# Optimization experiments

Measured on AMD Instinct MI355X. Metric: run time of the kernel, lower is better.

Reference implementation:

```python
import jax, jax.numpy as jnp
import numpy as np
from jax import lax

IN_C, OUT_C, K, Z_DIM, GROUPS = 256, 256, 3, 64, 1
B, H, W = 16, 32, 32


def setup_inputs() -> dict:
    key = jax.random.key(0)
    k1, k2, k3 = jax.random.split(key, 3)
    x = jax.random.normal(k1, (B, IN_C, H, W), dtype=jnp.float32)
    z = jax.random.normal(k2, (B, Z_DIM), dtype=jnp.float32)
    # nn.Linear(z_dim, groups*out_per_group*in_per_group*k*k, bias=False).weight
    fan = GROUPS * (OUT_C // GROUPS) * (IN_C // GROUPS) * K * K  # 589824
    w_lin = jax.random.normal(k3, (fan, Z_DIM), dtype=jnp.float32) * (1.0 / np.sqrt(Z_DIM))
    return {"x": x, "z": z, "w_lin": w_lin}


def reference(x, z, w_lin):
    b = x.shape[0]
    in_per_group = IN_C // GROUPS
    # hypernetwork: per-sample conv weights [B, out_c, in_c/groups, k, k]
    Wgen = (z @ w_lin.T).reshape(b, OUT_C, in_per_group, K, K)
    pad = K // 2

    def conv_one(xi, Wi):
        # xi: [in_c, H, W], Wi: [out_c, in_c/groups, k, k]
        y = lax.conv_general_dilated(
            xi[None], Wi,
            window_strides=(1, 1),
            padding=[(pad, pad), (pad, pad)],
            dimension_numbers=("NCHW", "OIHW", "NCHW"),
            feature_group_count=GROUPS,
        )
        return y[0]

    return jax.vmap(conv_one)(x, Wgen)  # [B, out_c, H, W]
```

## Files before the change

kernel.cpp:

```cpp
#include <hip/hip_runtime.h>

#define PB_ 589824
#define XT_PB 295936
#define XGR 544

typedef __bf16 bf16;
typedef __bf16 bf16x4 __attribute__((ext_vector_type(4)));
typedef __bf16 bf16x8 __attribute__((ext_vector_type(8)));
typedef float f32x4 __attribute__((ext_vector_type(4)));

static __device__ inline bf16x8 cvt8(float4 a, float4 b) {
  bf16x8 r;
  r[0] = (bf16)a.x; r[1] = (bf16)a.y; r[2] = (bf16)a.z; r[3] = (bf16)a.w;
  r[4] = (bf16)b.x; r[5] = (bf16)b.y; r[6] = (bf16)b.z; r[7] = (bf16)b.w;
  return r;
}

__global__ __launch_bounds__(256) void prep_kernel(const float* __restrict__ z,
                                                   const float* __restrict__ wl,
                                                   const float* __restrict__ x,
                                                   bf16* __restrict__ WgA,
                                                   bf16* __restrict__ xt) {
  const int bid = blockIdx.x;
  if (bid < 1152) {
    __shared__ __align__(16) char wsm[16384];
    const int c_  = bid & 7;
    const int tap = (bid >> 3) % 9;
    const int ob  = bid / 72;
    const int lane = threadIdx.x & 63;
    const int wave = threadIdx.x >> 6;
    const int l15 = lane & 15;
    const int q = lane >> 4;

    const float* zp = z + l15 * 64 + q * 8;
    bf16x8 bz[2];
#pragma unroll
    for (int kc = 0; kc < 2; ++kc)
      bz[kc] = cvt8(*(const float4*)(zp + kc * 32), *(const float4*)(zp + kc * 32 + 4));

#pragma unroll
    for (int mi = 0; mi < 4; ++mi) {
      const int m = wave * 4 + mi;
#pragma unroll
      for (int h = 0; h < 2; ++h) {
        const long t = (long)(ob * 16 + m) * 2304 + (c_ * 32 + h * 16 + l15) * 9 + tap;
        const float* wp = wl + t * 64 + q * 8;
        f32x4 acc = {0.f, 0.f, 0.f, 0.f};
#pragma unroll
        for (int kc = 0; kc < 2; ++kc) {
          bf16x8 aw = cvt8(*(const float4*)(wp + kc * 32), *(const float4*)(wp + kc * 32 + 4));
          acc = __builtin_amdgcn_mfma_f32_16x16x32_bf16(aw, bz[kc], acc, 0, 0, 0);
        }
        bf16x4 o;
        o[0] = (bf16)acc[0]; o[1] = (bf16)acc[1]; o[2] = (bf16)acc[2]; o[3] = (bf16)acc[3];
        const int elem = ((h * 2 + (q >> 1)) * 16 + m) * 8 + (q & 1) * 4;
        int byte = (l15 << 10) + elem * 2;
        byte ^= (l15 & 7) << 4;
        *(bf16x4*)(wsm + byte) = o;
      }
    }
    __syncthreads();
    const int b = threadIdx.x >> 4;
    const int l16 = threadIdx.x & 15;
    const long gbase = ((((long)b * 16 + ob) * 9 + tap) * 8 + c_) * 512;
#pragma unroll
    for (int i = 0; i < 4; ++i) {
      int byte = (b << 10) + (l16 << 4) + (i << 8);
      byte ^= (b & 7) << 4;
      uint4 v = *(const uint4*)(wsm + byte);
      *(uint4*)(WgA + gbase + l16 * 8 + i * 128) = v;
    }
  } else if (bid < 1416) {
    int g = (bid - 1152) * 256 + threadIdx.x;
    int b = g / 4224;
    int rem = g - b * 4224;
    int pi = rem >> 5;
    int gq = rem & 31;
    int p;
    if (pi < 34) p = pi;
    else if (pi < 68) p = 1122 + (pi - 34);
    else {
      int k = (pi - 68) >> 1;
      p = (k + 1) * 34 + (((pi - 68) & 1) ? 33 : 0);
    }
    *(uint4*)(xt + (long)b * XT_PB + p * 256 + gq * 8) = make_uint4(0u, 0u, 0u, 0u);
  } else {
    __shared__ bf16 tile[32][33];
    int i = bid - 1416;
    int row = i & 31, c0 = ((i >> 5) & 7) * 32, b = i >> 8;
    int l = threadIdx.x & 31;
    int r = threadIdx.x >> 5;
#pragma unroll
    for (int j = 0; j < 4; ++j) {
      int ch = r + j * 8;
      tile[ch][l] = (bf16)x[((b * 256 + c0 + ch) * 1024) + row * 32 + l];
    }
    __syncthreads();
#pragma unroll
    for (int j = 0; j < 4; ++j) {
      int col = r + j * 8;
      xt[(long)b * XT_PB + ((row + 1) * 34 + (col + 1)) * 256 + c0 + l] = tile[l][col];
    }
  }
}

__global__ __launch_bounds__(256, 4) void conv_kernel(const bf16* __restrict__ WgA,
                                                      const bf16* __restrict__ xt,
                                                      float* __restrict__ y) {
  __shared__ __align__(16) bf16 xs[2][XGR * 8];
  const int id = blockIdx.x;
  const int xcd = id & 7;
  const int k = id >> 3;
  const int b = ((k & 1) << 3) | xcd;
  const int r2 = k >> 1;
  const int mt = r2 & 3;
  const int nt = r2 >> 2;
  const int tid = threadIdx.x;
  const int lane = tid & 63;
  const int wave = tid >> 6;
  const int wm = wave & 1;
  const int wn = wave >> 1;
  const int l15 = lane & 15;
  const int q = lane >> 4;
  const int oc0 = mt * 64;

  const bf16* xtb = xt + (long)b * XT_PB;
  const bf16* xstage = xtb + (nt * 2) * 34 * 256;
  const bf16* Wb = WgA + (long)b * PB_;

  f32x4 acc[2][2] = {};

#define STAGE(IC0, SEL)                                                          \
  for (int g0 = wave * 64; g0 < XGR; g0 += 256) {                                \
    int g = g0 + lane;                                                           \
    int pix = g >> 2, slot = g & 3;                                              \
    int qq = slot ^ ((pix >> 1) & 3);                                            \
    if (g < XGR) {                                                               \
      const bf16* src = xstage + (pix * 256 + (IC0) + qq * 8);                   \
      __builtin_amdgcn_global_load_lds(                                          \
          (const __attribute__((address_space(1))) void*)src,                    \
          (__attribute__((address_space(3))) void*)(&xs[SEL][g0 * 8]), 16, 0, 0);\
    }                                                                            \
  }

  STAGE(0, 0)
  for (int c = 0; c < 8; ++c) {
    __syncthreads();
    if (c < 7) { STAGE((c + 1) * 32, (c + 1) & 1) }
    const bf16* buf = &xs[c & 1][0];
#pragma unroll
    for (int tap = 0; tap < 9; ++tap) {
      const int kh = tap / 3, kw = tap % 3;
      bf16x8 afr[2];
#pragma unroll
      for (int mi = 0; mi < 2; ++mi) {
        const int ob = (oc0 >> 4) + wm * 2 + mi;
        afr[mi] = *(const bf16x8*)(Wb + (((ob * 9 + tap) * 8 + c) * 512 + lane * 8));
      }
      bf16x8 bfr[2];
#pragma unroll
      for (int n = 0; n < 2; ++n) {
        int pl = wn * 32 + n * 16;
        int pr = pl >> 5;
        int pc = (pl & 31) + l15;
        int spix = (pr + kh) * 34 + pc + kw;
        bfr[n] = *(const bf16x8*)(buf + spix * 32 + ((((spix >> 1) & 3) ^ q) * 8));
      }
#pragma unroll
      for (int mi = 0; mi < 2; ++mi)
#pragma unroll
        for (int n = 0; n < 2; ++n)
          acc[mi][n] = __builtin_amdgcn_mfma_f32_16x16x32_bf16(afr[mi], bfr[n],
                                                               acc[mi][n], 0, 0, 0);
    }
  }

#pragma unroll
  for (int mi = 0; mi < 2; ++mi) {
    int ocb = oc0 + (wm * 2 + mi) * 16 + q * 4;
#pragma unroll
    for (int n = 0; n < 2; ++n) {
      int p = nt * 64 + wn * 32 + n * 16 + l15;
      float* yp = y + ((long)b * 256 + ocb) * 1024 + p;
#pragma unroll
      for (int rr = 0; rr < 4; ++rr)
        yp[rr * 1024] = acc[mi][n][rr];
    }
  }
#undef STAGE
}

extern "C" void kernel_launch(void* const* d_in, const int* in_sizes, int n_in,
                              void* d_out, int out_size, void* d_ws, size_t ws_size,
                              hipStream_t stream) {
  const float* x  = (const float*)d_in[0];
  const float* z  = (const float*)d_in[1];
  const float* wl = (const float*)d_in[2];
  float* y = (float*)d_out;
  bf16* WgA = (bf16*)d_ws;
  bf16* xt  = (bf16*)((char*)d_ws + 18874368);

  prep_kernel<<<5512, 256, 0, stream>>>(z, wl, x, WgA, xt);
  conv_kernel<<<1024, 256, 0, stream>>>(WgA, xt, y);
}
```

Before: 261.7 us.

## Fuse prep and conv into a persistent kernel with a grid-wide barrier

Merges the weight-generation and input-transpose prep kernel with the convolution kernel into one persistent launch of 1024 blocks. The blocks loop over the prep work items, meet at an atomic-counter grid barrier, then each runs its conv tile. This is meant to remove the second kernel launch and the tail gap between the two kernels. It adds a tiny zero-counter launch and a spin barrier, which deadlocks if all 1024 blocks cannot be resident at once. It also cuts prep parallelism from 5512 blocks to 1024 looping blocks.

```diff
diff --git a/kernel.cpp b/kernel.cpp
--- a/kernel.cpp
+++ b/kernel.cpp
@@ -3,6 +3,9 @@
 #define PB_ 589824
 #define XT_PB 295936
 #define XGR 544
+#define NBLK 1024
+#define NPREP 5512
+#define CTR_OFF 28344320
 
 typedef __bf16 bf16;
 typedef __bf16 bf16x4 __attribute__((ext_vector_type(4)));
@@ -16,178 +19,193 @@
   return r;
 }
 
-__global__ __launch_bounds__(256) void prep_kernel(const float* __restrict__ z,
-                                                   const float* __restrict__ wl,
-                                                   const float* __restrict__ x,
-                                                   bf16* __restrict__ WgA,
-                                                   bf16* __restrict__ xt) {
-  const int bid = blockIdx.x;
-  if (bid < 1152) {
-    __shared__ __align__(16) char wsm[16384];
-    const int c_  = bid & 7;
-    const int tap = (bid >> 3) % 9;
-    const int ob  = bid / 72;
-    const int lane = threadIdx.x & 63;
-    const int wave = threadIdx.x >> 6;
+__global__ void zero_ctr(unsigned* c) { *c = 0u; }
+
+__global__ __launch_bounds__(256, 4) void fused_kernel(const float* __restrict__ z,
+                                                       const float* __restrict__ wl,
+                                                       const float* __restrict__ x,
+                                                       bf16* __restrict__ WgA,
+                                                       bf16* __restrict__ xt,
+                                                       float* __restrict__ y,
+                                                       unsigned* __restrict__ ctr) {
+  __shared__ __align__(16) char smem[17408];
+  const int g = blockIdx.x;
+  const int tid = threadIdx.x;
+
+  for (int u = g; u < NPREP; u += NBLK) {
+    if (u < 1152) {
+      char* wsm = smem;
+      const int c_  = u & 7;
+      const int tap = (u >> 3) % 9;
+      const int ob  = u / 72;
+      const int lane = tid & 63;
+      const int wave = tid >> 6;
+      const int l15 = lane & 15;
+      const int q = lane >> 4;
+
+      const float* zp = z + l15 * 64 + q * 8;
+      bf16x8 bz[2];
+#pragma unroll
+      for (int kc = 0; kc < 2; ++kc)
+        bz[kc] = cvt8(*(const float4*)(zp + kc * 32), *(const float4*)(zp + kc * 32 + 4));
+
+#pragma unroll
+      for (int mi = 0; mi < 4; ++mi) {
+        const int m = wave * 4 + mi;
+#pragma unroll
+        for (int h = 0; h < 2; ++h) {
+          const long t = (long)(ob * 16 + m) * 2304 + (c_ * 32 + h * 16 + l15) * 9 + tap;
+          const float* wp = wl + t * 64 + q * 8;
+          f32x4 acc = {0.f, 0.f, 0.f, 0.f};
+#pragma unroll
+          for (int kc = 0; kc < 2; ++kc) {
+            bf16x8 aw = cvt8(*(const float4*)(wp + kc * 32), *(const float4*)(wp + kc * 32 + 4));
+            acc = __builtin_amdgcn_mfma_f32_16x16x32_bf16(aw, bz[kc], acc, 0, 0, 0);
+          }
+          bf16x4 o;
+          o[0] = (bf16)acc[0]; o[1] = (bf16)acc[1]; o[2] = (bf16)acc[2]; o[3] = (bf16)acc[3];
+          const int elem = ((h * 2 + (q >> 1)) * 16 + m) * 8 + (q & 1) * 4;
+          int byte = (l15 << 10) + elem * 2;
+          byte ^= (l15 & 7) << 4;
+          *(bf16x4*)(wsm + byte) = o;
+        }
+      }
+      __syncthreads();
+      const int bb = tid >> 4;
+      const int l16 = tid & 15;
+      const long gbase = ((((long)bb * 16 + ob) * 9 + tap) * 8 + c_) * 512;
+#pragma unroll
+      for (int i = 0; i < 4; ++i) {
+        int byte = (bb << 10) + (l16 << 4) + (i << 8);
+        byte ^= (bb & 7) << 4;
+        uint4 v = *(const uint4*)(wsm + byte);
+        *(uint4*)(WgA + gbase + l16 * 8 + i * 128) = v;
+      }
+    } else if (u < 1416) {
+      int gg = (u - 1152) * 256 + tid;
+      int b = gg / 4224;
+      int rem = gg - b * 4224;
+      int pi = rem >> 5;
+      int gq = rem & 31;
+      int p;
+      if (pi < 34) p = pi;
+      else if (pi < 68) p = 1122 + (pi - 34);
+      else {
+        int kk = (pi - 68) >> 1;
+        p = (kk + 1) * 34 + (((pi - 68) & 1) ? 33 : 0);
+      }
+      *(uint4*)(xt + (long)b * XT_PB + p * 256 + gq * 8) = make_uint4(0u, 0u, 0u, 0u);
+    } else {
+      bf16(*tile)[33] = (bf16(*)[33])smem;
+      int i = u - 1416;
+      int row = i & 31, c0 = ((i >> 5) & 7) * 32, b = i >> 8;
+      int l = tid & 31;
+      int r = tid >> 5;
+#pragma unroll
+      for (int j = 0; j < 4; ++j) {
+        int ch = r + j * 8;
+        tile[ch][l] = (bf16)x[((b * 256 + c0 + ch) * 1024) + row * 32 + l];
+      }
+      __syncthreads();
+#pragma unroll
+      for (int j = 0; j < 4; ++j) {
+        int col = r + j * 8;
+        xt[(long)b * XT_PB + ((row + 1) * 34 + (col + 1)) * 256 + c0 + l] = tile[l][col];
+      }
+    }
+    __syncthreads();
+  }
+
+  if (tid == 0) {
+    __hip_atomic_fetch_add(ctr, 1u, __ATOMIC_RELEASE, __HIP_MEMORY_SCOPE_AGENT);
+    while (__hip_atomic_load(ctr, __ATOMIC_ACQUIRE, __HIP_MEMORY_SCOPE_AGENT) < NBLK)
+      __builtin_amdgcn_s_sleep(16);
+  }
+  __syncthreads();
+
+  {
+    bf16* xsb = (bf16*)smem;
+    const int id = g;
+    const int xcd = id & 7;
+    const int k = id >> 3;
+    const int b = ((k & 1) << 3) | xcd;
+    const int r2 = k >> 1;
+    const int mt = r2 & 3;
+    const int nt = r2 >> 2;
+    const int lane = tid & 63;
+    const int wave = tid >> 6;
+    const int wm = wave & 1;
+    const int wn = wave >> 1;
     const int l15 = lane & 15;
     const int q = lane >> 4;
-
-    const float* zp = z + l15 * 64 + q * 8;
-    bf16x8 bz[2];
-#pragma unroll
-    for (int kc = 0; kc < 2; ++kc)
-      bz[kc] = cvt8(*(const float4*)(zp + kc * 32), *(const float4*)(zp + kc * 32 + 4));
-
-#pragma unroll
-    for (int mi = 0; mi < 4; ++mi) {
-      const int m = wave * 4 + mi;
-#pragma unroll
-      for (int h = 0; h < 2; ++h) {
-        const long t = (long)(ob * 16 + m) * 2304 + (c_ * 32 + h * 16 + l15) * 9 + tap;
-        const float* wp = wl + t * 64 + q * 8;
-        f32x4 acc = {0.f, 0.f, 0.f, 0.f};
-#pragma unroll
-        for (int kc = 0; kc < 2; ++kc) {
-          bf16x8 aw = cvt8(*(const float4*)(wp + kc * 32), *(const float4*)(wp + kc * 32 + 4));
-          acc = __builtin_amdgcn_mfma_f32_16x16x32_bf16(aw, bz[kc], acc, 0, 0, 0);
-        }
-        bf16x4 o;
-        o[0] = (bf16)acc[0]; o[1] = (bf16)acc[1]; o[2] = (bf16)acc[2]; o[3] = (bf16)acc[3];
-        const int elem = ((h * 2 + (q >> 1)) * 16 + m) * 8 + (q & 1) * 4;
-        int byte = (l15 << 10) + elem * 2;
-        byte ^= (l15 & 7) << 4;
-        *(bf16x4*)(wsm + byte) = o;
-      }
-    }
-    __syncthreads();
-    const int b = threadIdx.x >> 4;
-    const int l16 = threadIdx.x & 15;
-    const long gbase = ((((long)b * 16 + ob) * 9 + tap) * 8 + c_) * 512;
-#pragma unroll
-    for (int i = 0; i < 4; ++i) {
-      int byte = (b << 10) + (l16 << 4) + (i << 8);
-      byte ^= (b & 7) << 4;
-      uint4 v = *(const uint4*)(wsm + byte);
-      *(uint4*)(WgA + gbase + l16 * 8 + i * 128) = v;
-    }
-  } else if (bid < 1416) {
-    int g = (bid - 1152) * 256 + threadIdx.x;
-    int b = g / 4224;
-    int rem = g - b * 4224;
-    int pi = rem >> 5;
-    int gq = rem & 31;
-    int p;
-    if (pi < 34) p = pi;
-    else if (pi < 68) p = 1122 + (pi - 34);
-    else {
-      int k = (pi - 68) >> 1;
-      p = (k + 1) * 34 + (((pi - 68) & 1) ? 33 : 0);
-    }
-    *(uint4*)(xt + (long)b * XT_PB + p * 256 + gq * 8) = make_uint4(0u, 0u, 0u, 0u);
-  } else {
-    __shared__ bf16 tile[32][33];
-    int i = bid - 1416;
-    int row = i & 31, c0 = ((i >> 5) & 7) * 32, b = i >> 8;
-    int l = threadIdx.x & 31;
-    int r = threadIdx.x >> 5;
-#pragma unroll
-    for (int j = 0; j < 4; ++j) {
-      int ch = r + j * 8;
-      tile[ch][l] = (bf16)x[((b * 256 + c0 + ch) * 1024) + row * 32 + l];
-    }
-    __syncthreads();
-#pragma unroll
-    for (int j = 0; j < 4; ++j) {
-      int col = r + j * 8;
-      xt[(long)b * XT_PB + ((row + 1) * 34 + (col + 1)) * 256 + c0 + l] = tile[l][col];
-    }
-  }
-}
-
-__global__ __launch_bounds__(256, 4) void conv_kernel(const bf16* __restrict__ WgA,
-                                                      const bf16* __restrict__ xt,
-                                                      float* __restrict__ y) {
-  __shared__ __align__(16) bf16 xs[2][XGR * 8];
-  const int id = blockIdx.x;
-  const int xcd = id & 7;
-  const int k = id >> 3;
-  const int b = ((k & 1) << 3) | xcd;
-  const int r2 = k >> 1;
-  const int mt = r2 & 3;
-  const int nt = r2 >> 2;
-  const int tid = threadIdx.x;
-  const int lane = tid & 63;
-  const int wave = tid >> 6;
-  const int wm = wave & 1;
-  const int wn = wave >> 1;
-  const int l15 = lane & 15;
-  const int q = lane >> 4;
-  const int oc0 = mt * 64;
-
-  const bf16* xtb = xt + (long)b * XT_PB;
-  const bf16* xstage = xtb + (nt * 2) * 34 * 256;
-  const bf16* Wb = WgA + (long)b * PB_;
-
-  f32x4 acc[2][2] = {};
+    const int oc0 = mt * 64;
+
+    const bf16* xtb = xt + (long)b * XT_PB;
+    const bf16* xstage = xtb + (nt * 2) * 34 * 256;
+    const bf16* Wb = WgA + (long)b * PB_;
+
+    f32x4 acc[2][2] = {};
 
 #define STAGE(IC0, SEL)                                                          \
   for (int g0 = wave * 64; g0 < XGR; g0 += 256) {                                \
-    int g = g0 + lane;                                                           \
-    int pix = g >> 2, slot = g & 3;                                              \
+    int gg = g0 + lane;                                                          \
+    int pix = gg >> 2, slot = gg & 3;                                            \
     int qq = slot ^ ((pix >> 1) & 3);                                            \
-    if (g < XGR) {                                                               \
+    if (gg < XGR) {                                                              \
       const bf16* src = xstage + (pix * 256 + (IC0) + qq * 8);                   \
       __builtin_amdgcn_global_load_lds(                                          \
           (const __attribute__((address_space(1))) void*)src,                    \
-          (__attribute__((address_space(3))) void*)(&xs[SEL][g0 * 8]), 16, 0, 0);\
+          (__attribute__((address_space(3))) void*)(xsb + (SEL) * (XGR * 8) +    \
+                                                   g0 * 8), 16, 0, 0);           \
     }                                                                            \
   }
 
-  STAGE(0, 0)
-  for (int c = 0; c < 8; ++c) {
-    __syncthreads();
-    if (c < 7) { STAGE((c + 1) * 32, (c + 1) & 1) }
-    const bf16* buf = &xs[c & 1][0];
-#pragma unroll
-    for (int tap = 0; tap < 9; ++tap) {
-      const int kh = tap / 3, kw = tap % 3;
-      bf16x8 afr[2];
-#pragma unroll
-      for (int mi = 0; mi < 2; ++mi) {
-        const int ob = (oc0 >> 4) + wm * 2 + mi;
-        afr[mi] = *(const bf16x8*)(Wb + (((ob * 9 + tap) * 8 + c) * 512 + lane * 8));
-      }
-      bf16x8 bfr[2];
+    STAGE(0, 0)
+    for (int c = 0; c < 8; ++c) {
+      __syncthreads();
+      if (c < 7) { STAGE((c + 1) * 32, (c + 1) & 1) }
+      const bf16* buf = xsb + (c & 1) * (XGR * 8);
+#pragma unroll
+      for (int tap = 0; tap < 9; ++tap) {
+        const int kh = tap / 3, kw = tap % 3;
+        bf16x8 afr[2];
+#pragma unroll
+        for (int mi = 0; mi < 2; ++mi) {
+          const int ob = (oc0 >> 4) + wm * 2 + mi;
+          afr[mi] = *(const bf16x8*)(Wb + (((ob * 9 + tap) * 8 + c) * 512 + lane * 8));
+        }
+        bf16x8 bfr[2];
+#pragma unroll
+        for (int n = 0; n < 2; ++n) {
+          int pl = wn * 32 + n * 16;
+          int pr = pl >> 5;
+          int pc = (pl & 31) + l15;
+          int spix = (pr + kh) * 34 + pc + kw;
+          bfr[n] = *(const bf16x8*)(buf + spix * 32 + ((((spix >> 1) & 3) ^ q) * 8));
+        }
+#pragma unroll
+        for (int mi = 0; mi < 2; ++mi)
+#pragma unroll
+          for (int n = 0; n < 2; ++n)
+            acc[mi][n] = __builtin_amdgcn_mfma_f32_16x16x32_bf16(afr[mi], bfr[n],
+                                                                 acc[mi][n], 0, 0, 0);
+      }
+    }
+
+#pragma unroll
+    for (int mi = 0; mi < 2; ++mi) {
+      int ocb = oc0 + (wm * 2 + mi) * 16 + q * 4;
 #pragma unroll
       for (int n = 0; n < 2; ++n) {
-        int pl = wn * 32 + n * 16;
-        int pr = pl >> 5;
-        int pc = (pl & 31) + l15;
-        int spix = (pr + kh) * 34 + pc + kw;
-        bfr[n] = *(const bf16x8*)(buf + spix * 32 + ((((spix >> 1) & 3) ^ q) * 8));
-      }
-#pragma unroll
-      for (int mi = 0; mi < 2; ++mi)
-#pragma unroll
-        for (int n = 0; n < 2; ++n)
-          acc[mi][n] = __builtin_amdgcn_mfma_f32_16x16x32_bf16(afr[mi], bfr[n],
-                                                               acc[mi][n], 0, 0, 0);
+        int p = nt * 64 + wn * 32 + n * 16 + l15;
+        float* yp = y + ((long)b * 256 + ocb) * 1024 + p;
+#pragma unroll
+        for (int rr = 0; rr < 4; ++rr)
+          yp[rr * 1024] = acc[mi][n][rr];
+      }
     }
-  }
-
-#pragma unroll
-  for (int mi = 0; mi < 2; ++mi) {
-    int ocb = oc0 + (wm * 2 + mi) * 16 + q * 4;
-#pragma unroll
-    for (int n = 0; n < 2; ++n) {
-      int p = nt * 64 + wn * 32 + n * 16 + l15;
-      float* yp = y + ((long)b * 256 + ocb) * 1024 + p;
-#pragma unroll
-      for (int rr = 0; rr < 4; ++rr)
-        yp[rr * 1024] = acc[mi][n][rr];
-    }
-  }
 #undef STAGE
+  }
 }
 
 extern "C" void kernel_launch(void* const* d_in, const int* in_sizes, int n_in,
@@ -199,7 +217,8 @@
   float* y = (float*)d_out;
   bf16* WgA = (bf16*)d_ws;
   bf16* xt  = (bf16*)((char*)d_ws + 18874368);
-
-  prep_kernel<<<5512, 256, 0, stream>>>(z, wl, x, WgA, xt);
-  conv_kernel<<<1024, 256, 0, stream>>>(WgA, xt, y);
+  unsigned* ctr = (unsigned*)((char*)d_ws + CTR_OFF);
+
+  zero_ctr<<<1, 1, 0, stream>>>(ctr);
+  fused_kernel<<<NBLK, 256, 0, stream>>>(z, wl, x, WgA, xt, y, ctr);
 }
```

Result: slower. 418.4 us (+59.9%).

## Double-buffer weight fragments in registers, prefetching next kernel row during MFMAs

Applied to the files above, without the earlier changes.

Restructures the conv inner loop into per-kernel-row steps with a two-slot register buffer of A (weight) fragments, so the global loads for the next row (or the next channel chunk's first row) are issued before the current row's MFMAs run. The channel loop is unrolled by two so buffer slots alternate statically. This aims to hide global-memory latency of the per-sample weight loads behind compute, at the cost of more VGPRs (12 bf16x8 fragments live), which may pressure the 4-waves-per-SIMD launch bound.

```diff
diff --git a/kernel.cpp b/kernel.cpp
--- a/kernel.cpp
+++ b/kernel.cpp
@@ -127,8 +127,20 @@
   const bf16* xtb = xt + (long)b * XT_PB;
   const bf16* xstage = xtb + (nt * 2) * 34 * 256;
   const bf16* Wb = WgA + (long)b * PB_;
+  const bf16* Wlane = Wb + (long)((oc0 >> 4) + wm * 2) * 9 * 8 * 512 + lane * 8;
 
   f32x4 acc[2][2] = {};
+  bf16x8 afr[2][3][2];
+
+#define LOADA(KH, C, SLOT)                                                       \
+  {                                                                              \
+    _Pragma("unroll")                                                            \
+    for (int kw_ = 0; kw_ < 3; ++kw_)                                            \
+      _Pragma("unroll")                                                          \
+      for (int mi_ = 0; mi_ < 2; ++mi_)                                          \
+        afr[SLOT][kw_][mi_] = *(const bf16x8*)(                                  \
+            Wlane + (long)(((mi_ * 9 + (KH) * 3 + kw_) * 8 + (C)) * 512));       \
+  }
 
 #define STAGE(IC0, SEL)                                                          \
   for (int g0 = wave * 64; g0 < XGR; g0 += 256) {                                \
@@ -143,35 +155,51 @@
     }                                                                            \
   }
 
+#define ROW(KH, SLOT, BUF, PF)                                                   \
+  {                                                                              \
+    PF                                                                           \
+    _Pragma("unroll")                                                            \
+    for (int kw = 0; kw < 3; ++kw) {                                             \
+      bf16x8 bfr[2];                                                             \
+      _Pragma("unroll")                                                          \
+      for (int n = 0; n < 2; ++n) {                                              \
+        int pl = wn * 32 + n * 16;                                               \
+        int pr = pl >> 5;                                                        \
+        int pc = (pl & 31) + l15;                                                \
+        int spix = (pr + (KH)) * 34 + pc + kw;                                   \
+        bfr[n] = *(const bf16x8*)((BUF) + spix * 32 +                            \
+                                  ((((spix >> 1) & 3) ^ q) * 8));                \
+      }                                                                          \
+      _Pragma("unroll")                                                          \
+      for (int mi = 0; mi < 2; ++mi)                                             \
+        _Pragma("unroll")                                                        \
+        for (int n = 0; n < 2; ++n)                                              \
+          acc[mi][n] = __builtin_amdgcn_mfma_f32_16x16x32_bf16(                  \
+              afr[SLOT][kw][mi], bfr[n], acc[mi][n], 0, 0, 0);                   \
+    }                                                                            \
+  }
+
   STAGE(0, 0)
-  for (int c = 0; c < 8; ++c) {
-    __syncthreads();
-    if (c < 7) { STAGE((c + 1) * 32, (c + 1) & 1) }
-    const bf16* buf = &xs[c & 1][0];
-#pragma unroll
-    for (int tap = 0; tap < 9; ++tap) {
-      const int kh = tap / 3, kw = tap % 3;
-      bf16x8 afr[2];
-#pragma unroll
-      for (int mi = 0; mi < 2; ++mi) {
-        const int ob = (oc0 >> 4) + wm * 2 + mi;
-        afr[mi] = *(const bf16x8*)(Wb + (((ob * 9 + tap) * 8 + c) * 512 + lane * 8));
-      }
-      bf16x8 bfr[2];
-#pragma unroll
-      for (int n = 0; n < 2; ++n) {
-        int pl = wn * 32 + n * 16;
-        int pr = pl >> 5;
-        int pc = (pl & 31) + l15;
-        int spix = (pr + kh) * 34 + pc + kw;
-        bfr[n] = *(const bf16x8*)(buf + spix * 32 + ((((spix >> 1) & 3) ^ q) * 8));
-      }
-#pragma unroll
-      for (int mi = 0; mi < 2; ++mi)
-#pragma unroll
-        for (int n = 0; n < 2; ++n)
-          acc[mi][n] = __builtin_amdgcn_mfma_f32_16x16x32_bf16(afr[mi], bfr[n],
-                                                               acc[mi][n], 0, 0, 0);
+  LOADA(0, 0, 0)
+  for (int c2 = 0; c2 < 4; ++c2) {
+    const int ce = c2 * 2;
+    {
+      __syncthreads();
+      STAGE((ce + 1) * 32, (ce + 1) & 1)
+      const bf16* buf = &xs[ce & 1][0];
+      ROW(0, 0, buf, LOADA(1, ce, 1))
+      ROW(1, 1, buf, LOADA(2, ce, 0))
+      ROW(2, 0, buf, LOADA(0, ce + 1, 1))
+    }
+    {
+      const int co = ce + 1;
+      __syncthreads();
+      if (co < 7) { STAGE((co + 1) * 32, (co + 1) & 1) }
+      const bf16* buf = &xs[co & 1][0];
+      ROW(0, 1, buf, LOADA(1, co, 0))
+      ROW(1, 0, buf, LOADA(2, co, 1))
+      if (co < 7) { ROW(2, 1, buf, LOADA(0, co + 1, 0)) }
+      else        { ROW(2, 1, buf, ) }
     }
   }
 
@@ -188,6 +216,8 @@
     }
   }
 #undef STAGE
+#undef LOADA
+#undef ROW
 }
 
 extern "C" void kernel_launch(void* const* d_in, const int* in_sizes, int n_in,
```

After: 269.5 us. 1.03x slower.
